# Performance work log

Measured on AMD Instinct MI355X. Metric: run time of the kernel, lower is better.

Reference implementation:

```python
import jax, jax.numpy as jnp
import numpy as np

B, T, F, H, D, L = 64, 1024, 304, 304, 128, 128  # batch, enc len, feat=emb, hidden, dict_size, max_phn_num


def _init(k, sh):
    bound = 1.0 / np.sqrt(H)
    return jax.random.uniform(k, sh, jnp.float32, -bound, bound)


def setup_inputs() -> dict:
    key = jax.random.key(0)
    ks = jax.random.split(key, 12)
    return {
        "x": jax.random.normal(ks[0], (B, T, F), jnp.float32),
        "target": jax.random.randint(ks[1], (B, L, 1), 0, D),
        "emb": jax.random.normal(ks[2], (D, F), jnp.float32),
        "enc_Wih": _init(ks[3], (3 * H, F)),
        "enc_Whh": _init(ks[4], (3 * H, H)),
        "enc_bih": _init(ks[5], (3 * H,)),
        "enc_bhh": _init(ks[6], (3 * H,)),
        "dec_Wih": _init(ks[7], (3 * H, F)),
        "dec_Whh": _init(ks[8], (3 * H, H)),
        "dec_bih": _init(ks[9], (3 * H,)),
        "dec_bhh": _init(ks[10], (3 * H,)),
        "lin_W": _init(ks[11], (D, H)),
        "lin_b": jnp.zeros((D,), jnp.float32),
    }


def gru_step(h, xt, Wih, Whh, bih, bhh):
    # PyTorch GRU cell, gate order (r, z, n)
    gi = xt @ Wih.T + bih            # [B, 3H]
    gh = h @ Whh.T + bhh             # [B, 3H]
    ir, iz, innew = jnp.split(gi, 3, axis=-1)
    hr, hz, hn = jnp.split(gh, 3, axis=-1)
    r = jax.nn.sigmoid(ir + hr)
    z = jax.nn.sigmoid(iz + hz)
    n = jnp.tanh(innew + r * hn)
    return (1.0 - z) * n + z * h


def reference(x, target, emb, enc_Wih, enc_Whh, enc_bih, enc_bhh,
              dec_Wih, dec_Whh, dec_bih, dec_bhh, lin_W, lin_b):
    Bsz = x.shape[0]
    Hdim = enc_Whh.shape[1]
    Lphn = target.shape[1]

    # ---- encoder GRU over acoustic frames ----
    h0 = jnp.zeros((Bsz, Hdim), x.dtype)

    def enc_scan(h, xt):
        return gru_step(h, xt, enc_Wih, enc_Whh, enc_bih, enc_bhh), None

    h_enc, _ = jax.lax.scan(enc_scan, h0, jnp.swapaxes(x, 0, 1))

    tok0 = target[:, 0, 0]  # [B]

    def dec_scan(carry, _):
        h, tok = carry
        e = emb[tok]                                   # [B, F]
        h = gru_step(h, e, dec_Wih, dec_Whh, dec_bih, dec_bhh)
        logits = h @ lin_W.T + lin_b                   # [B, D]
        nxt = jnp.argmax(logits, axis=-1)
        return (h, nxt), logits

    _, logits = jax.lax.scan(dec_scan, (h_enc, tok0), None, length=Lphn)
    softmaxs = jnp.swapaxes(logits, 0, 1)              # [B, L, D]

    softmax_cal = softmaxs[:, :-1, :].reshape(-1, softmaxs.shape[-1])
    target_cal = target[:, 1:, :].reshape(-1)
    asr_outputs = jnp.argmax(softmaxs[:, :-1, :], axis=2)[:, :, None]
    return softmax_cal, target_cal, asr_outputs
```

## Files before the change

kernel.cpp:

```cpp
#include <hip/hip_runtime.h>
#include <cstdint>
#include <cstddef>

#define HN 304
#define G3 912
#define US 76
#define RS 228
#define NB 64
#define TSTEPS 1024
#define LDEC 127
#define DCLS 128

#define OUT_O1 1040384
#define OUT_O2 1048512

static const size_t OFF_GI   = 0;
static const size_t OFF_HP   = 239075328ull;
static const size_t OFF_AM   = 239230976ull;
static const size_t OFF_ABRT = 239233024ull;
static const size_t OFF_TAB  = 239233280ull;
static const size_t WS_NEED  = 239700224ull;

__global__ __launch_bounds__(256) void gi_gemm(const float* __restrict__ X,
                                               const float* __restrict__ W,
                                               const float* __restrict__ bias,
                                               float* __restrict__ out)
{
    __shared__ float xs[16][68];
    __shared__ float wsm[16][68];
    const int tid = threadIdx.x;
    const int m0 = blockIdx.x * 64;
    const int n0 = blockIdx.y * 64;
    const int tx = tid & 15, ty = tid >> 4;
    const int lr = tid >> 2;
    const int lk = (tid & 3) * 4;
    float c[4][4];
#pragma unroll
    for (int i = 0; i < 4; ++i)
#pragma unroll
        for (int j = 0; j < 4; ++j) c[i][j] = 0.f;

    for (int k0 = 0; k0 < HN; k0 += 16) {
        float4 xv = *(const float4*)(X + (size_t)(m0 + lr) * HN + k0 + lk);
        float4 wv = make_float4(0.f, 0.f, 0.f, 0.f);
        if (n0 + lr < G3) wv = *(const float4*)(W + (size_t)(n0 + lr) * HN + k0 + lk);
        xs[lk + 0][lr] = xv.x; xs[lk + 1][lr] = xv.y; xs[lk + 2][lr] = xv.z; xs[lk + 3][lr] = xv.w;
        wsm[lk + 0][lr] = wv.x; wsm[lk + 1][lr] = wv.y; wsm[lk + 2][lr] = wv.z; wsm[lk + 3][lr] = wv.w;
        __syncthreads();
#pragma unroll
        for (int kk = 0; kk < 16; ++kk) {
            const float4 a4 = *(const float4*)&xs[kk][ty * 4];
            const float4 b4 = *(const float4*)&wsm[kk][tx * 4];
            c[0][0] += a4.x * b4.x; c[0][1] += a4.x * b4.y; c[0][2] += a4.x * b4.z; c[0][3] += a4.x * b4.w;
            c[1][0] += a4.y * b4.x; c[1][1] += a4.y * b4.y; c[1][2] += a4.y * b4.z; c[1][3] += a4.y * b4.w;
            c[2][0] += a4.z * b4.x; c[2][1] += a4.z * b4.y; c[2][2] += a4.z * b4.z; c[2][3] += a4.z * b4.w;
            c[3][0] += a4.w * b4.x; c[3][1] += a4.w * b4.y; c[3][2] += a4.w * b4.z; c[3][3] += a4.w * b4.w;
        }
        __syncthreads();
    }
#pragma unroll
    for (int i = 0; i < 4; ++i) {
        const int m = m0 + ty * 4 + i;
#pragma unroll
        for (int j = 0; j < 4; ++j) {
            const int n = n0 + tx * 4 + j;
            if (n < G3) out[(size_t)m * G3 + n] = c[i][j] + bias[n];
        }
    }
}

__global__ __launch_bounds__(256) void table_k(const float* __restrict__ emb,
                                               const float* __restrict__ Wih,
                                               const float* __restrict__ bih,
                                               float* __restrict__ tab)
{
    const int idx = blockIdx.x * 256 + threadIdx.x;
    const int d = idx / G3;
    const int R = idx - d * G3;
    const float4* e4 = (const float4*)(emb + (size_t)d * HN);
    const float4* w4 = (const float4*)(Wih + (size_t)R * HN);
    float acc = 0.f;
#pragma unroll
    for (int j = 0; j < 76; ++j) {
        const float4 e = e4[j], w = w4[j];
        acc += e.x * w.x; acc += e.y * w.y; acc += e.z * w.z; acc += e.w * w.w;
    }
    tab[idx] = acc + bih[R];
}

__global__ void tcal_k(const int* __restrict__ target, float* __restrict__ out)
{
    const int i = blockIdx.x * 256 + threadIdx.x;
    if (i < NB * LDEC) {
        const int b = i / LDEC;
        const int t = i - b * LDEC;
        out[OUT_O1 + i] = (float)target[b * 128 + t + 1];
    }
}

__device__ __forceinline__ unsigned poll_tag32(unsigned int* p, unsigned want, int* abortf)
{
    unsigned v; int g = 0;
    for (;;) {
        v = __hip_atomic_load(p, __ATOMIC_RELAXED, __HIP_MEMORY_SCOPE_AGENT);
        if ((v & 3u) == want) break;
        if ((++g & 255) == 0) {
            if (__hip_atomic_load(abortf, __ATOMIC_RELAXED, __HIP_MEMORY_SCOPE_AGENT) != 0) break;
            if (g > (1 << 19)) {
                __hip_atomic_store(abortf, 1, __ATOMIC_RELAXED, __HIP_MEMORY_SCOPE_AGENT);
                break;
            }
        }
    }
    __asm__ volatile("" ::: "memory");
    return v;
}

__device__ __forceinline__ unsigned long long spin_tag(unsigned long long* p, int want, int* abortf)
{
    int g = 0;
    unsigned long long r;
    for (;;) {
        r = __hip_atomic_load(p, __ATOMIC_RELAXED, __HIP_MEMORY_SCOPE_AGENT);
        if ((int)(r >> 32) >= want) break;
        if ((++g & 255) == 0) {
            if (__hip_atomic_load(abortf, __ATOMIC_RELAXED, __HIP_MEMORY_SCOPE_AGENT) != 0) break;
            if (g > (1 << 19)) {
                __hip_atomic_store(abortf, 1, __ATOMIC_RELAXED, __HIP_MEMORY_SCOPE_AGENT);
                break;
            }
        }
    }
    __asm__ volatile("" ::: "memory");
    return r;
}

__global__ __launch_bounds__(1024) void rnn_persist(
    const float* __restrict__ gi,
    const float* __restrict__ encWhh, const float* __restrict__ encBhh,
    const float* __restrict__ decWhh, const float* __restrict__ decBhh,
    const float* __restrict__ tab,
    const float* __restrict__ linW, const float* __restrict__ linB,
    const int* __restrict__ target,
    unsigned int* hpk, unsigned long long* amax, int* abortf, float* out)
{
    const int w = blockIdx.x;
    const int b = w & 63;
    const int s = w >> 6;
    const int tid = threadIdx.x;

    __shared__ alignas(16) float hbuf[HN];
    __shared__ alignas(16) float part[4][RS];
    __shared__ alignas(16) float lpart[32][9];
    __shared__ float logit_s[32];
    __shared__ float amx_v[4];
    __shared__ int   amx_i[4];

    const int ks = tid / RS;
    const int lr = tid - ks * RS;
    const bool comp = (tid < 912);
    const int g = lr / US;
    const int ul = lr - g * US;
    const int Rrow = g * HN + s * US + ul;
    const int u = s * US + tid;
    const int cq = tid / US;

    unsigned long long* amx = amax + b * 4;
    unsigned int* hpb = hpk + b * HN;

    float4 wreg[19];
    if (comp) {
        const float4* wp = (const float4*)(encWhh + (size_t)Rrow * HN + (size_t)ks * US);
#pragma unroll
        for (int j = 0; j < 19; ++j) wreg[j] = wp[j];
    }
    float b_r = 0.f, b_z = 0.f, b_n = 0.f;
    if (tid < US) { b_r = encBhh[u]; b_z = encBhh[HN + u]; b_n = encBhh[2 * HN + u]; }

    for (int i = tid; i < HN; i += 1024) hbuf[i] = 0.f;
    __syncthreads();

    const float* gib = gi + (size_t)b * TSTEPS * G3;

    for (int t = 0; t < TSTEPS; ++t) {
        const int T = t + 1;
        float gr = 0.f, gz = 0.f, gn = 0.f;
        if (tid < US) {
            const float* gp = gib + (size_t)t * G3;
            gr = gp[u]; gz = gp[HN + u]; gn = gp[2 * HN + u];
        }
        if (comp) {
            const float4* hp = (const float4*)(hbuf + ks * US);
            float acc = 0.f;
#pragma unroll
            for (int j = 0; j < 19; ++j) {
                const float4 h4 = hp[j], w4 = wreg[j];
                acc += w4.x * h4.x; acc += w4.y * h4.y; acc += w4.z * h4.z; acc += w4.w * h4.w;
            }
            part[ks][lr] = acc;
        }
        __syncthreads();
        if (tid < US) {
            const float ghr = part[0][tid] + part[1][tid] + part[2][tid] + part[3][tid] + b_r;
            const float ghz = part[0][US + tid] + part[1][US + tid] + part[2][US + tid] + part[3][US + tid] + b_z;
            const float ghn = part[0][2 * US + tid] + part[1][2 * US + tid] + part[2][2 * US + tid] + part[3][2 * US + tid] + b_n;
            const float r = 1.f / (1.f + expf(-(gr + ghr)));
            const float z = 1.f / (1.f + expf(-(gz + ghz)));
            const float n = tanhf(gn + r * ghn);
            const float hnew = (1.f - z) * n + z * hbuf[u];
            const unsigned hb = (__float_as_uint(hnew) & ~3u) | ((unsigned)T & 3u);
            hbuf[u] = __uint_as_float(hb);
            __hip_atomic_store(&hpb[(T & 1) * NB * HN + u], hb,
                               __ATOMIC_RELAXED, __HIP_MEMORY_SCOPE_AGENT);
        }
        if (tid < HN && cq != s) {
            const unsigned v = poll_tag32(&hpb[(T & 1) * NB * HN + tid],
                                          (unsigned)T & 3u, abortf);
            hbuf[tid] = __uint_as_float(v);
        }
        __syncthreads();
    }

    if (comp) {
        const float4* wp = (const float4*)(decWhh + (size_t)Rrow * HN + (size_t)ks * US);
#pragma unroll
        for (int j = 0; j < 19; ++j) wreg[j] = wp[j];
    }
    if (tid < US) { b_r = decBhh[u]; b_z = decBhh[HN + u]; b_n = decBhh[2 * HN + u]; }
    int tok = target[b * 128];
    const int lrow = tid >> 3;
    const int lks = tid & 7;
    __syncthreads();

    for (int t = 0; t < LDEC; ++t) {
        const int T = TSTEPS + 1 + t;
        float gr = 0.f, gz = 0.f, gn = 0.f;
        if (tid < US) {
            const float* tp = tab + (size_t)tok * G3;
            gr = tp[u]; gz = tp[HN + u]; gn = tp[2 * HN + u];
        }
        if (comp) {
            const float4* hp = (const float4*)(hbuf + ks * US);
            float acc = 0.f;
#pragma unroll
            for (int j = 0; j < 19; ++j) {
                const float4 h4 = hp[j], w4 = wreg[j];
                acc += w4.x * h4.x; acc += w4.y * h4.y; acc += w4.z * h4.z; acc += w4.w * h4.w;
            }
            part[ks][lr] = acc;
        }
        __syncthreads();
        if (tid < US) {
            const float ghr = part[0][tid] + part[1][tid] + part[2][tid] + part[3][tid] + b_r;
            const float ghz = part[0][US + tid] + part[1][US + tid] + part[2][US + tid] + part[3][US + tid] + b_z;
            const float ghn = part[0][2 * US + tid] + part[1][2 * US + tid] + part[2][2 * US + tid] + part[3][2 * US + tid] + b_n;
            const float r = 1.f / (1.f + expf(-(gr + ghr)));
            const float z = 1.f / (1.f + expf(-(gz + ghz)));
            const float n = tanhf(gn + r * ghn);
            const float hnew = (1.f - z) * n + z * hbuf[u];
            const unsigned hb = (__float_as_uint(hnew) & ~3u) | ((unsigned)T & 3u);
            hbuf[u] = __uint_as_float(hb);
            __hip_atomic_store(&hpb[(T & 1) * NB * HN + u], hb,
                               __ATOMIC_RELAXED, __HIP_MEMORY_SCOPE_AGENT);
        }
        if (tid < HN && cq != s) {
            const unsigned v = poll_tag32(&hpb[(T & 1) * NB * HN + tid],
                                          (unsigned)T & 3u, abortf);
            hbuf[tid] = __uint_as_float(v);
        }
        __syncthreads();

        if (tid < 256) {
            const float2* wl = (const float2*)(linW + (size_t)(s * 32 + lrow) * HN + (size_t)lks * 38);
            const float2* hl = (const float2*)(hbuf + lks * 38);
            float a = 0.f;
#pragma unroll
            for (int j = 0; j < 19; ++j) { const float2 wv = wl[j], hv = hl[j]; a += wv.x * hv.x; a += wv.y * hv.y; }
            lpart[lrow][lks] = a;
        }
        __syncthreads();
        if (tid < 32) {
            const float lg = lpart[tid][0] + lpart[tid][1] + lpart[tid][2] + lpart[tid][3]
                           + lpart[tid][4] + lpart[tid][5] + lpart[tid][6] + lpart[tid][7]
                           + linB[s * 32 + tid];
            logit_s[tid] = lg;
            out[((size_t)b * LDEC + t) * DCLS + s * 32 + tid] = lg;
        }
        __syncthreads();
        if (tid == 0) {
            float bv = logit_s[0]; int bi = 0;
            for (int i = 1; i < 32; ++i) { const float v = logit_s[i]; if (v > bv) { bv = v; bi = i; } }
            const unsigned tagf = (unsigned)(((t + 1) << 8) | (s * 32 + bi));
            const unsigned long long pk = ((unsigned long long)tagf << 32) | (unsigned long long)__float_as_uint(bv);
            __hip_atomic_store(&amx[s], pk, __ATOMIC_RELAXED, __HIP_MEMORY_SCOPE_AGENT);
        }
        if (tid < 4) {
            const unsigned long long r = spin_tag(&amx[tid], (t + 1) << 8, abortf);
            amx_v[tid] = __uint_as_float((unsigned)r);
            amx_i[tid] = (int)(r >> 32) & 255;
        }
        __syncthreads();
        {
            float gbv = amx_v[0]; int gbi = amx_i[0];
            if (amx_v[1] > gbv) { gbv = amx_v[1]; gbi = amx_i[1]; }
            if (amx_v[2] > gbv) { gbv = amx_v[2]; gbi = amx_i[2]; }
            if (amx_v[3] > gbv) { gbv = amx_v[3]; gbi = amx_i[3]; }
            tok = gbi;
            if (tid == 0 && s == 0) out[OUT_O2 + (size_t)b * LDEC + t] = (float)gbi;
        }
    }
}

extern "C" void kernel_launch(void* const* d_in, const int* in_sizes, int n_in,
                              void* d_out, int out_size, void* d_ws, size_t ws_size,
                              hipStream_t stream)
{
    (void)in_sizes; (void)n_in; (void)out_size;
    const float* x      = (const float*)d_in[0];
    const int*   target = (const int*)  d_in[1];
    const float* emb    = (const float*)d_in[2];
    const float* encWih = (const float*)d_in[3];
    const float* encWhh = (const float*)d_in[4];
    const float* encBih = (const float*)d_in[5];
    const float* encBhh = (const float*)d_in[6];
    const float* decWih = (const float*)d_in[7];
    const float* decWhh = (const float*)d_in[8];
    const float* decBih = (const float*)d_in[9];
    const float* decBhh = (const float*)d_in[10];
    const float* linW   = (const float*)d_in[11];
    const float* linB   = (const float*)d_in[12];
    float* out = (float*)d_out;
    char* ws = (char*)d_ws;

    if (ws_size < WS_NEED) return;

    float*              gi   = (float*)(ws + OFF_GI);
    unsigned int*       hpk  = (unsigned int*)(ws + OFF_HP);
    unsigned long long* amax = (unsigned long long*)(ws + OFF_AM);
    int*                abrt = (int*)(ws + OFF_ABRT);
    float*              tab  = (float*)(ws + OFF_TAB);

    hipMemsetAsync(ws + OFF_HP, 0, OFF_TAB - OFF_HP, stream);
    gi_gemm<<<dim3(1024, 15), 256, 0, stream>>>(x, encWih, encBih, gi);
    table_k<<<456, 256, 0, stream>>>(emb, decWih, decBih, tab);
    tcal_k<<<32, 256, 0, stream>>>(target, out);
    rnn_persist<<<256, 1024, 0, stream>>>(gi, encWhh, encBhh, decWhh, decBhh, tab,
                                          linW, linB, target, hpk, amax, abrt, out);
}
```

Baseline: 3.331 ms.

## Prefetch GEMM tiles and gate inputs, pipeline polls, overlap decoder argmax

The GI GEMM now loads the next K-tile into registers while computing on the current shared-memory tile. The encoder loads the next step's precomputed input gates one iteration ahead. The hidden-state poll keeps three outstanding atomic loads in flight to cut spin latency. In the decoder, the cross-block argmax wait moves to spare threads at the start of the next step, where it overlaps the recurrent matvec, and one barrier per step is dropped. The costs are extra register pressure and a trailing argmax gather after the loop.

Result: slower. 3.513 ms (+5.5%).

```diff
diff --git a/kernel.cpp b/kernel.cpp
--- a/kernel.cpp
+++ b/kernel.cpp
@@ -40,13 +40,19 @@
 #pragma unroll
         for (int j = 0; j < 4; ++j) c[i][j] = 0.f;
 
+    const bool wok = (n0 + lr < G3);
+    float4 xv = *(const float4*)(X + (size_t)(m0 + lr) * HN + lk);
+    float4 wv = wok ? *(const float4*)(W + (size_t)(n0 + lr) * HN + lk)
+                    : make_float4(0.f, 0.f, 0.f, 0.f);
+
     for (int k0 = 0; k0 < HN; k0 += 16) {
-        float4 xv = *(const float4*)(X + (size_t)(m0 + lr) * HN + k0 + lk);
-        float4 wv = make_float4(0.f, 0.f, 0.f, 0.f);
-        if (n0 + lr < G3) wv = *(const float4*)(W + (size_t)(n0 + lr) * HN + k0 + lk);
         xs[lk + 0][lr] = xv.x; xs[lk + 1][lr] = xv.y; xs[lk + 2][lr] = xv.z; xs[lk + 3][lr] = xv.w;
         wsm[lk + 0][lr] = wv.x; wsm[lk + 1][lr] = wv.y; wsm[lk + 2][lr] = wv.z; wsm[lk + 3][lr] = wv.w;
         __syncthreads();
+        if (k0 + 16 < HN) {
+            xv = *(const float4*)(X + (size_t)(m0 + lr) * HN + k0 + 16 + lk);
+            if (wok) wv = *(const float4*)(W + (size_t)(n0 + lr) * HN + k0 + 16 + lk);
+        }
 #pragma unroll
         for (int kk = 0; kk < 16; ++kk) {
             const float4 a4 = *(const float4*)&xs[kk][ty * 4];
@@ -98,12 +104,15 @@
     }
 }
 
-__device__ __forceinline__ unsigned poll_tag32(unsigned int* p, unsigned want, int* abortf)
-{
-    unsigned v; int g = 0;
-    for (;;) {
-        v = __hip_atomic_load(p, __ATOMIC_RELAXED, __HIP_MEMORY_SCOPE_AGENT);
-        if ((v & 3u) == want) break;
+__device__ __forceinline__ unsigned poll_tag32p(unsigned int* p, unsigned want, int* abortf)
+{
+    unsigned v0 = __hip_atomic_load(p, __ATOMIC_RELAXED, __HIP_MEMORY_SCOPE_AGENT);
+    unsigned v1 = __hip_atomic_load(p, __ATOMIC_RELAXED, __HIP_MEMORY_SCOPE_AGENT);
+    unsigned v2 = __hip_atomic_load(p, __ATOMIC_RELAXED, __HIP_MEMORY_SCOPE_AGENT);
+    int g = 0;
+    while ((v0 & 3u) != want) {
+        v0 = v1; v1 = v2;
+        v2 = __hip_atomic_load(p, __ATOMIC_RELAXED, __HIP_MEMORY_SCOPE_AGENT);
         if ((++g & 255) == 0) {
             if (__hip_atomic_load(abortf, __ATOMIC_RELAXED, __HIP_MEMORY_SCOPE_AGENT) != 0) break;
             if (g > (1 << 19)) {
@@ -113,7 +122,7 @@
         }
     }
     __asm__ volatile("" ::: "memory");
-    return v;
+    return v0;
 }
 
 __device__ __forceinline__ unsigned long long spin_tag(unsigned long long* p, int want, int* abortf)
@@ -155,6 +164,7 @@
     __shared__ float logit_s[32];
     __shared__ float amx_v[4];
     __shared__ int   amx_i[4];
+    __shared__ int   tok_s;
 
     const int ks = tid / RS;
     const int lr = tid - ks * RS;
@@ -182,12 +192,15 @@
 
     const float* gib = gi + (size_t)b * TSTEPS * G3;
 
+    float gr = 0.f, gz = 0.f, gn = 0.f;
+    if (tid < US) { gr = gib[u]; gz = gib[HN + u]; gn = gib[2 * HN + u]; }
+
     for (int t = 0; t < TSTEPS; ++t) {
         const int T = t + 1;
-        float gr = 0.f, gz = 0.f, gn = 0.f;
-        if (tid < US) {
-            const float* gp = gib + (size_t)t * G3;
-            gr = gp[u]; gz = gp[HN + u]; gn = gp[2 * HN + u];
+        float grn = 0.f, gzn = 0.f, gnn = 0.f;
+        if (tid < US && t + 1 < TSTEPS) {
+            const float* gp = gib + (size_t)(t + 1) * G3;
+            grn = gp[u]; gzn = gp[HN + u]; gnn = gp[2 * HN + u];
         }
         if (comp) {
             const float4* hp = (const float4*)(hbuf + ks * US);
@@ -214,11 +227,12 @@
                                __ATOMIC_RELAXED, __HIP_MEMORY_SCOPE_AGENT);
         }
         if (tid < HN && cq != s) {
-            const unsigned v = poll_tag32(&hpb[(T & 1) * NB * HN + tid],
-                                          (unsigned)T & 3u, abortf);
+            const unsigned v = poll_tag32p(&hpb[(T & 1) * NB * HN + tid],
+                                           (unsigned)T & 3u, abortf);
             hbuf[tid] = __uint_as_float(v);
         }
         __syncthreads();
+        gr = grn; gz = gzn; gn = gnn;
     }
 
     if (comp) {
@@ -227,17 +241,27 @@
         for (int j = 0; j < 19; ++j) wreg[j] = wp[j];
     }
     if (tid < US) { b_r = decBhh[u]; b_z = decBhh[HN + u]; b_n = decBhh[2 * HN + u]; }
-    int tok = target[b * 128];
+    const int tok0 = target[b * 128];
     const int lrow = tid >> 3;
     const int lks = tid & 7;
     __syncthreads();
 
     for (int t = 0; t < LDEC; ++t) {
         const int T = TSTEPS + 1 + t;
-        float gr = 0.f, gz = 0.f, gn = 0.f;
-        if (tid < US) {
-            const float* tp = tab + (size_t)tok * G3;
-            gr = tp[u]; gz = tp[HN + u]; gn = tp[2 * HN + u];
+
+        if (t > 0 && tid >= 960 && tid < 964) {
+            const int q = tid - 960;
+            const unsigned long long r = spin_tag(&amx[q], t << 8, abortf);
+            amx_v[q] = __uint_as_float((unsigned)r);
+            amx_i[q] = (int)(r >> 32) & 255;
+            if (q == 0) {
+                float gbv = amx_v[0]; int gbi = amx_i[0];
+                if (amx_v[1] > gbv) { gbv = amx_v[1]; gbi = amx_i[1]; }
+                if (amx_v[2] > gbv) { gbv = amx_v[2]; gbi = amx_i[2]; }
+                if (amx_v[3] > gbv) { gbv = amx_v[3]; gbi = amx_i[3]; }
+                tok_s = gbi;
+                if (s == 0) out[OUT_O2 + (size_t)b * LDEC + (t - 1)] = (float)gbi;
+            }
         }
         if (comp) {
             const float4* hp = (const float4*)(hbuf + ks * US);
@@ -251,12 +275,15 @@
         }
         __syncthreads();
         if (tid < US) {
+            const int tk = (t == 0) ? tok0 : tok_s;
+            const float* tp = tab + (size_t)tk * G3;
+            const float dgr = tp[u], dgz = tp[HN + u], dgn = tp[2 * HN + u];
             const float ghr = part[0][tid] + part[1][tid] + part[2][tid] + part[3][tid] + b_r;
             const float ghz = part[0][US + tid] + part[1][US + tid] + part[2][US + tid] + part[3][US + tid] + b_z;
             const float ghn = part[0][2 * US + tid] + part[1][2 * US + tid] + part[2][2 * US + tid] + part[3][2 * US + tid] + b_n;
-            const float r = 1.f / (1.f + expf(-(gr + ghr)));
-            const float z = 1.f / (1.f + expf(-(gz + ghz)));
-            const float n = tanhf(gn + r * ghn);
+            const float r = 1.f / (1.f + expf(-(dgr + ghr)));
+            const float z = 1.f / (1.f + expf(-(dgz + ghz)));
+            const float n = tanhf(dgn + r * ghn);
             const float hnew = (1.f - z) * n + z * hbuf[u];
             const unsigned hb = (__float_as_uint(hnew) & ~3u) | ((unsigned)T & 3u);
             hbuf[u] = __uint_as_float(hb);
@@ -264,8 +291,8 @@
                                __ATOMIC_RELAXED, __HIP_MEMORY_SCOPE_AGENT);
         }
         if (tid < HN && cq != s) {
-            const unsigned v = poll_tag32(&hpb[(T & 1) * NB * HN + tid],
-                                          (unsigned)T & 3u, abortf);
+            const unsigned v = poll_tag32p(&hpb[(T & 1) * NB * HN + tid],
+                                           (unsigned)T & 3u, abortf);
             hbuf[tid] = __uint_as_float(v);
         }
         __syncthreads();
@@ -294,20 +321,17 @@
             const unsigned long long pk = ((unsigned long long)tagf << 32) | (unsigned long long)__float_as_uint(bv);
             __hip_atomic_store(&amx[s], pk, __ATOMIC_RELAXED, __HIP_MEMORY_SCOPE_AGENT);
         }
-        if (tid < 4) {
-            const unsigned long long r = spin_tag(&amx[tid], (t + 1) << 8, abortf);
-            amx_v[tid] = __uint_as_float((unsigned)r);
-            amx_i[tid] = (int)(r >> 32) & 255;
-        }
-        __syncthreads();
-        {
-            float gbv = amx_v[0]; int gbi = amx_i[0];
-            if (amx_v[1] > gbv) { gbv = amx_v[1]; gbi = amx_i[1]; }
-            if (amx_v[2] > gbv) { gbv = amx_v[2]; gbi = amx_i[2]; }
-            if (amx_v[3] > gbv) { gbv = amx_v[3]; gbi = amx_i[3]; }
-            tok = gbi;
-            if (tid == 0 && s == 0) out[OUT_O2 + (size_t)b * LDEC + t] = (float)gbi;
-        }
+    }
+
+    if (s == 0 && tid == 0) {
+        float gbv = 0.f; int gbi = 0;
+        for (int q = 0; q < 4; ++q) {
+            const unsigned long long r = spin_tag(&amx[q], LDEC << 8, abortf);
+            const float v = __uint_as_float((unsigned)r);
+            const int ii = (int)(r >> 32) & 255;
+            if (q == 0 || v > gbv) { gbv = v; gbi = ii; }
+        }
+        out[OUT_O2 + (size_t)b * LDEC + (LDEC - 1)] = (float)gbi;
     }
 }
 
```

## Halve recurrent block size with two rows per thread; prefetch GEMM tiles

Applied to the files above, without the earlier changes.

The persistent GRU kernel now launches 512 threads per block instead of 1024. Each compute thread holds two weight rows in registers and produces two partial dot products per step, which means fewer waves take part in every per-step barrier. The input-projection GEMM also loads the next K-tile into registers while the current tile is being computed, to hide global load latency. The cost is higher register use and a longer serial FMA chain per thread in the latency-bound recurrent step. The unseen logits and argmax code must still be correct with only 512 threads.

Measured after the change: 3.143 ms. 1.06x faster.

```diff
diff --git a/kernel.cpp b/kernel.cpp
--- a/kernel.cpp
+++ b/kernel.cpp
@@ -40,13 +40,19 @@
 #pragma unroll
         for (int j = 0; j < 4; ++j) c[i][j] = 0.f;
 
+    const bool wok = (n0 + lr < G3);
+    float4 xv = *(const float4*)(X + (size_t)(m0 + lr) * HN + lk);
+    float4 wv = wok ? *(const float4*)(W + (size_t)(n0 + lr) * HN + lk)
+                    : make_float4(0.f, 0.f, 0.f, 0.f);
+
     for (int k0 = 0; k0 < HN; k0 += 16) {
-        float4 xv = *(const float4*)(X + (size_t)(m0 + lr) * HN + k0 + lk);
-        float4 wv = make_float4(0.f, 0.f, 0.f, 0.f);
-        if (n0 + lr < G3) wv = *(const float4*)(W + (size_t)(n0 + lr) * HN + k0 + lk);
         xs[lk + 0][lr] = xv.x; xs[lk + 1][lr] = xv.y; xs[lk + 2][lr] = xv.z; xs[lk + 3][lr] = xv.w;
         wsm[lk + 0][lr] = wv.x; wsm[lk + 1][lr] = wv.y; wsm[lk + 2][lr] = wv.z; wsm[lk + 3][lr] = wv.w;
         __syncthreads();
+        if (k0 + 16 < HN) {
+            xv = *(const float4*)(X + (size_t)(m0 + lr) * HN + k0 + 16 + lk);
+            if (wok) wv = *(const float4*)(W + (size_t)(n0 + lr) * HN + k0 + 16 + lk);
+        }
 #pragma unroll
         for (int kk = 0; kk < 16; ++kk) {
             const float4 a4 = *(const float4*)&xs[kk][ty * 4];
@@ -135,7 +141,7 @@
     return r;
 }
 
-__global__ __launch_bounds__(1024) void rnn_persist(
+__global__ __launch_bounds__(512, 2) void rnn_persist(
     const float* __restrict__ gi,
     const float* __restrict__ encWhh, const float* __restrict__ encBhh,
     const float* __restrict__ decWhh, const float* __restrict__ decBhh,
@@ -156,28 +162,30 @@
     __shared__ float amx_v[4];
     __shared__ int   amx_i[4];
 
-    const int ks = tid / RS;
-    const int lr = tid - ks * RS;
-    const bool comp = (tid < 912);
-    const int g = lr / US;
-    const int ul = lr - g * US;
-    const int Rrow = g * HN + s * US + ul;
+    const bool comp = (tid < 456);
+    const int ksq = tid / 114;
+    const int lp  = tid - ksq * 114;
+    const int g0 = lp / US,        ul0 = lp - g0 * US;
+    const int g1 = (lp + 114) / US, ul1 = (lp + 114) - g1 * US;
+    const int Rrow0 = g0 * HN + s * US + ul0;
+    const int Rrow1 = g1 * HN + s * US + ul1;
     const int u = s * US + tid;
     const int cq = tid / US;
 
     unsigned long long* amx = amax + b * 4;
     unsigned int* hpb = hpk + b * HN;
 
-    float4 wreg[19];
+    float4 wreg0[19], wreg1[19];
     if (comp) {
-        const float4* wp = (const float4*)(encWhh + (size_t)Rrow * HN + (size_t)ks * US);
-#pragma unroll
-        for (int j = 0; j < 19; ++j) wreg[j] = wp[j];
+        const float4* wp0 = (const float4*)(encWhh + (size_t)Rrow0 * HN + (size_t)ksq * US);
+        const float4* wp1 = (const float4*)(encWhh + (size_t)Rrow1 * HN + (size_t)ksq * US);
+#pragma unroll
+        for (int j = 0; j < 19; ++j) { wreg0[j] = wp0[j]; wreg1[j] = wp1[j]; }
     }
     float b_r = 0.f, b_z = 0.f, b_n = 0.f;
     if (tid < US) { b_r = encBhh[u]; b_z = encBhh[HN + u]; b_n = encBhh[2 * HN + u]; }
 
-    for (int i = tid; i < HN; i += 1024) hbuf[i] = 0.f;
+    for (int i = tid; i < HN; i += 512) hbuf[i] = 0.f;
     __syncthreads();
 
     const float* gib = gi + (size_t)b * TSTEPS * G3;
@@ -190,14 +198,17 @@
             gr = gp[u]; gz = gp[HN + u]; gn = gp[2 * HN + u];
         }
         if (comp) {
-            const float4* hp = (const float4*)(hbuf + ks * US);
-            float acc = 0.f;
+            const float4* hp = (const float4*)(hbuf + ksq * US);
+            float acc0 = 0.f, acc1 = 0.f;
 #pragma unroll
             for (int j = 0; j < 19; ++j) {
-                const float4 h4 = hp[j], w4 = wreg[j];
-                acc += w4.x * h4.x; acc += w4.y * h4.y; acc += w4.z * h4.z; acc += w4.w * h4.w;
+                const float4 h4 = hp[j];
+                const float4 w0 = wreg0[j], w1 = wreg1[j];
+                acc0 += w0.x * h4.x; acc0 += w0.y * h4.y; acc0 += w0.z * h4.z; acc0 += w0.w * h4.w;
+                acc1 += w1.x * h4.x; acc1 += w1.y * h4.y; acc1 += w1.z * h4.z; acc1 += w1.w * h4.w;
             }
-            part[ks][lr] = acc;
+            part[ksq][lp] = acc0;
+            part[ksq][lp + 114] = acc1;
         }
         __syncthreads();
         if (tid < US) {
@@ -222,9 +233,10 @@
     }
 
     if (comp) {
-        const float4* wp = (const float4*)(decWhh + (size_t)Rrow * HN + (size_t)ks * US);
-#pragma unroll
-        for (int j = 0; j < 19; ++j) wreg[j] = wp[j];
+        const float4* wp0 = (const float4*)(decWhh + (size_t)Rrow0 * HN + (size_t)ksq * US);
+        const float4* wp1 = (const float4*)(decWhh + (size_t)Rrow1 * HN + (size_t)ksq * US);
+#pragma unroll
+        for (int j = 0; j < 19; ++j) { wreg0[j] = wp0[j]; wreg1[j] = wp1[j]; }
     }
     if (tid < US) { b_r = decBhh[u]; b_z = decBhh[HN + u]; b_n = decBhh[2 * HN + u]; }
     int tok = target[b * 128];
@@ -240,14 +252,17 @@
             gr = tp[u]; gz = tp[HN + u]; gn = tp[2 * HN + u];
         }
         if (comp) {
-            const float4* hp = (const float4*)(hbuf + ks * US);
-            float acc = 0.f;
+            const float4* hp = (const float4*)(hbuf + ksq * US);
+            float acc0 = 0.f, acc1 = 0.f;
 #pragma unroll
             for (int j = 0; j < 19; ++j) {
-                const float4 h4 = hp[j], w4 = wreg[j];
-                acc += w4.x * h4.x; acc += w4.y * h4.y; acc += w4.z * h4.z; acc += w4.w * h4.w;
+                const float4 h4 = hp[j];
+                const float4 w0 = wreg0[j], w1 = wreg1[j];
+                acc0 += w0.x * h4.x; acc0 += w0.y * h4.y; acc0 += w0.z * h4.z; acc0 += w0.w * h4.w;
+                acc1 += w1.x * h4.x; acc1 += w1.y * h4.y; acc1 += w1.z * h4.z; acc1 += w1.w * h4.w;
             }
-            part[ks][lr] = acc;
+            part[ksq][lp] = acc0;
+            part[ksq][lp + 114] = acc1;
         }
         __syncthreads();
         if (tid < US) {
@@ -344,6 +359,6 @@
     gi_gemm<<<dim3(1024, 15), 256, 0, stream>>>(x, encWih, encBih, gi);
     table_k<<<456, 256, 0, stream>>>(emb, decWih, decBih, tab);
     tcal_k<<<32, 256, 0, stream>>>(target, out);
-    rnn_persist<<<256, 1024, 0, stream>>>(gi, encWhh, encBhh, decWhh, decBhh, tab,
-                                          linW, linB, target, hpk, amax, abrt, out);
-}
+    rnn_persist<<<256, 512, 0, stream>>>(gi, encWhh, encBhh, decWhh, decBhh, tab,
+                                         linW, linB, target, hpk, amax, abrt, out);
+}
```
